# Performance work log

Hardware: AMD Instinct MI355X
Metric: run time of the kernel (lower is better)

Reference implementation:

```python
import jax, jax.numpy as jnp
import numpy as np

N, E, H, FN, FE, L = 100000, 600000, 128, 64, 16, 4


def setup_inputs() -> dict:
    key = jax.random.key(0)
    ks = jax.random.split(key, 16)
    s = 0.05
    return {
        "node_feats": jax.random.normal(ks[0], (N, FN), jnp.float32),
        "edge_feats": jax.random.normal(ks[1], (E, FE), jnp.float32),
        "src": jax.random.randint(ks[2], (E,), 0, N),
        "dst": jax.random.randint(ks[3], (E,), 0, N),
        # node projection
        "Wn": jax.random.normal(ks[4], (FN, H), jnp.float32) * s,
        "bn": jnp.zeros((H,), jnp.float32),
        # edge MLP: Linear -> ReLU -> Linear
        "We1": jax.random.normal(ks[5], (FE, H), jnp.float32) * s,
        "be1": jnp.zeros((H,), jnp.float32),
        "We2": jax.random.normal(ks[6], (H, H), jnp.float32) * s,
        "be2": jnp.zeros((H,), jnp.float32),
        # per-layer GINE apply MLPs: Linear -> ReLU -> Linear, stacked over L layers
        "W1": jax.random.normal(ks[7], (L, H, H), jnp.float32) * s,
        "b1": jnp.zeros((L, H), jnp.float32),
        "W2": jax.random.normal(ks[8], (L, H, H), jnp.float32) * s,
        "b2": jnp.zeros((L, H), jnp.float32),
    }


def reference(node_feats, edge_feats, src, dst, Wn, bn, We1, be1, We2, be2, W1, b1, W2, b2):
    relu = jax.nn.relu
    # initial node projection + ReLU
    h = relu(node_feats @ Wn + bn)                     # [N, H]
    # edge feature MLP
    e = relu(edge_feats @ We1 + be1) @ We2 + be2       # [E, H]
    n_nodes = h.shape[0]
    for l in range(W1.shape[0]):
        # GINEConv (eps = 0): message = relu(h[src] + e), sum-aggregate at dst
        m = relu(h[src] + e)                           # [E, H] gather + combine
        agg = jax.ops.segment_sum(m, dst, num_segments=n_nodes)  # [N, H] scatter-add
        z = h + agg                                    # (1+eps)*h + agg, eps=0
        z = relu(z @ W1[l] + b1[l]) @ W2[l] + b2[l]    # apply MLP
        h = relu(z)                                    # outer ReLU in forward loop
    return h
```

## Files before the change

### kernel.cpp

```cpp
#include <hip/hip_runtime.h>

#define BLK 256

typedef short bf16x8 __attribute__((ext_vector_type(8)));
typedef float f32x4 __attribute__((ext_vector_type(4)));

__device__ __forceinline__ unsigned short f2bf(float f) {
    unsigned int u = __float_as_uint(f);
    u += 0x7FFFu + ((u >> 16) & 1u);
    return (unsigned short)(u >> 16);
}
__device__ __forceinline__ float bf2f(unsigned short s) {
    return __uint_as_float(((unsigned int)s) << 16);
}

__global__ __launch_bounds__(BLK) void prep_w(
    const float* __restrict__ Wn, const float* __restrict__ We1,
    const float* __restrict__ We2, const float* __restrict__ W1,
    const float* __restrict__ W2, unsigned short* __restrict__ wp)
{
    const int slot = blockIdx.y;
    const int K = (slot == 9) ? 64 : (slot == 10) ? 32 : 128;
    const int i = blockIdx.x * BLK + threadIdx.x;
    if (i >= K * 128) return;
    const int k = i >> 7, n = i & 127;
    float f;
    if (slot == 0)      f = We2[k * 128 + n];
    else if (slot <= 4) f = W1[(size_t)(slot - 1) * 16384 + k * 128 + n];
    else if (slot <= 8) f = W2[(size_t)(slot - 5) * 16384 + k * 128 + n];
    else if (slot == 9) f = Wn[k * 128 + n];
    else                f = (k < 16) ? We1[k * 128 + n] : 0.f;
    const unsigned short hi = f2bf(f);
    const unsigned short lo = f2bf(f - bf2f(hi));
    const int mask = (slot == 10) ? 3 : 7;
    const int idx = n * K + (k ^ ((n & mask) << 3));
    unsigned short* base = wp + (size_t)slot * 32768;
    base[idx] = hi;
    base[K * 128 + idx] = lo;
}

template <int KDIM, int A_BF16, int OUT_BF16>
__global__ __launch_bounds__(BLK) void gemm128(
    const void* __restrict__ Av, const unsigned short* __restrict__ Wp,
    const float* __restrict__ bias, void* __restrict__ outv,
    int M, int do_relu)
{
    __shared__ unsigned short Bl[2 * KDIM * 128];
    const int tid = threadIdx.x;
    {
        const float4* s = (const float4*)Wp;
        float4* d = (float4*)Bl;
        #pragma unroll
        for (int i = 0; i < KDIM / 8; ++i) d[tid + i * BLK] = s[tid + i * BLK];
    }
    __syncthreads();

    const int lane = tid & 63;
    const int wv   = tid >> 6;
    const int l15  = lane & 15;
    const int g    = lane >> 4;
    const int wbase = wv * 32;
    const int NKS = KDIM / 32;

    float bcol[8];
    #pragma unroll
    for (int cf = 0; cf < 8; ++cf) bcol[cf] = bias[cf * 16 + l15];

    const int ntiles = (M + 127) >> 7;
    for (int tile = blockIdx.x; tile < ntiles; tile += gridDim.x) {
        bf16x8 af[2][KDIM / 32];
        #pragma unroll
        for (int rf = 0; rf < 2; ++rf) {
            const int row = tile * 128 + wbase + rf * 16 + l15;
            const bool ok = row < M;
            #pragma unroll
            for (int ks = 0; ks < NKS; ++ks) {
                const int k0 = ks * 32 + g * 8;
                if (A_BF16) {
                    af[rf][ks] = ok
                        ? *(const bf16x8*)((const unsigned short*)Av + (size_t)row * KDIM + k0)
                        : (bf16x8)0;
                } else {
                    if (ok) {
                        const float* ap = (const float*)Av + (size_t)row * KDIM + k0;
                        const float4 f0 = *(const float4*)(ap);
                        const float4 f1 = *(const float4*)(ap + 4);
                        bf16x8 a;
                        a[0] = (short)f2bf(f0.x); a[1] = (short)f2bf(f0.y);
                        a[2] = (short)f2bf(f0.z); a[3] = (short)f2bf(f0.w);
                        a[4] = (short)f2bf(f1.x); a[5] = (short)f2bf(f1.y);
                        a[6] = (short)f2bf(f1.z); a[7] = (short)f2bf(f1.w);
                        af[rf][ks] = a;
                    } else af[rf][ks] = (bf16x8)0;
                }
            }
        }
        f32x4 acc[2][8];
        #pragma unroll
        for (int rf = 0; rf < 2; ++rf)
            #pragma unroll
            for (int cf = 0; cf < 8; ++cf) {
                const float b = bcol[cf];
                acc[rf][cf][0] = b; acc[rf][cf][1] = b;
                acc[rf][cf][2] = b; acc[rf][cf][3] = b;
            }
        #pragma unroll
        for (int ks = 0; ks < NKS; ++ks) {
            #pragma unroll
            for (int cf = 0; cf < 8; ++cf) {
                const int c = cf * 16 + l15;
                const int ku = (ks * 32 + g * 8) ^ ((c & 7) << 3);
                const bf16x8 bh = *(const bf16x8*)(&Bl[c * KDIM + ku]);
                const bf16x8 blo = *(const bf16x8*)(&Bl[KDIM * 128 + c * KDIM + ku]);
                acc[0][cf] = __builtin_amdgcn_mfma_f32_16x16x32_bf16(af[0][ks], bh, acc[0][cf], 0, 0, 0);
                acc[1][cf] = __builtin_amdgcn_mfma_f32_16x16x32_bf16(af[1][ks], bh, acc[1][cf], 0, 0, 0);
                acc[0][cf] = __builtin_amdgcn_mfma_f32_16x16x32_bf16(af[0][ks], blo, acc[0][cf], 0, 0, 0);
                acc[1][cf] = __builtin_amdgcn_mfma_f32_16x16x32_bf16(af[1][ks], blo, acc[1][cf], 0, 0, 0);
            }
        }
        #pragma unroll
        for (int rf = 0; rf < 2; ++rf) {
            const int r0 = tile * 128 + wbase + rf * 16 + g * 4;
            #pragma unroll
            for (int cf = 0; cf < 8; ++cf) {
                const int col = cf * 16 + l15;
                const f32x4 v = acc[rf][cf];
                #pragma unroll
                for (int j = 0; j < 4; ++j) {
                    const int row = r0 + j;
                    if (row < M) {
                        float x = v[j];
                        if (do_relu) x = fmaxf(x, 0.f);
                        if (OUT_BF16)
                            ((unsigned short*)outv)[(size_t)row * 128 + col] = f2bf(x);
                        else
                            ((float*)outv)[(size_t)row * 128 + col] = x;
                    }
                }
            }
        }
    }
}

__global__ __launch_bounds__(BLK) void edge_mlp(
    const float* __restrict__ ef, const unsigned short* __restrict__ w1p,
    const unsigned short* __restrict__ w2p, const float* __restrict__ be1,
    const float* __restrict__ be2, unsigned short* __restrict__ out, int M)
{
    __shared__ unsigned short B1[2 * 32 * 128];
    __shared__ unsigned short B2[128 * 128];
    __shared__ unsigned short stg[4][16 * 128];
    const int tid = threadIdx.x;
    {
        const float4* s1 = (const float4*)w1p;
        float4* d1 = (float4*)B1;
        #pragma unroll
        for (int i = 0; i < 4; ++i) d1[tid + i * BLK] = s1[tid + i * BLK];
        const float4* s2 = (const float4*)w2p;
        float4* d2 = (float4*)B2;
        #pragma unroll
        for (int i = 0; i < 8; ++i) d2[tid + i * BLK] = s2[tid + i * BLK];
    }
    __syncthreads();

    const int lane = tid & 63;
    const int wv   = tid >> 6;
    const int l15  = lane & 15;
    const int g    = lane >> 4;
    const int wbase = wv * 32;

    float bcol1[8], bcol2[8];
    #pragma unroll
    for (int cf = 0; cf < 8; ++cf) {
        bcol1[cf] = be1[cf * 16 + l15];
        bcol2[cf] = be2[cf * 16 + l15];
    }

    const int ntiles = (M + 127) >> 7;
    for (int tile = blockIdx.x; tile < ntiles; tile += gridDim.x) {
        #pragma unroll
        for (int rf = 0; rf < 2; ++rf) {
            const int row = tile * 128 + wbase + rf * 16 + l15;
            const bool ok = row < M;
            bf16x8 a1 = (bf16x8)0;
            if (g < 2 && ok) {
                const float* ap = ef + (size_t)row * 16 + g * 8;
                const float4 f0 = *(const float4*)(ap);
                const float4 f1 = *(const float4*)(ap + 4);
                a1[0] = (short)f2bf(f0.x); a1[1] = (short)f2bf(f0.y);
                a1[2] = (short)f2bf(f0.z); a1[3] = (short)f2bf(f0.w);
                a1[4] = (short)f2bf(f1.x); a1[5] = (short)f2bf(f1.y);
                a1[6] = (short)f2bf(f1.z); a1[7] = (short)f2bf(f1.w);
            }
            f32x4 acc1[8];
            #pragma unroll
            for (int cf = 0; cf < 8; ++cf) {
                const float b = bcol1[cf];
                acc1[cf][0] = b; acc1[cf][1] = b; acc1[cf][2] = b; acc1[cf][3] = b;
            }
            #pragma unroll
            for (int cf = 0; cf < 8; ++cf) {
                const int c = cf * 16 + l15;
                const int ku = (g * 8) ^ ((c & 3) << 3);
                const bf16x8 bh  = *(const bf16x8*)(&B1[c * 32 + ku]);
                const bf16x8 blo = *(const bf16x8*)(&B1[4096 + c * 32 + ku]);
                acc1[cf] = __builtin_amdgcn_mfma_f32_16x16x32_bf16(a1, bh,  acc1[cf], 0, 0, 0);
                acc1[cf] = __builtin_amdgcn_mfma_f32_16x16x32_bf16(a1, blo, acc1[cf], 0, 0, 0);
            }
            #pragma unroll
            for (int cf = 0; cf < 8; ++cf) {
                const int col = cf * 16 + l15;
                #pragma unroll
                for (int j = 0; j < 4; ++j) {
                    const int rl = g * 4 + j;
                    stg[wv][rl * 128 + (col ^ ((rl & 7) << 3))] =
                        f2bf(fmaxf(acc1[cf][j], 0.f));
                }
            }
            __syncthreads();
            bf16x8 a2[4];
            #pragma unroll
            for (int ks = 0; ks < 4; ++ks) {
                const int k0 = ks * 32 + g * 8;
                a2[ks] = *(const bf16x8*)(&stg[wv][l15 * 128 + (k0 ^ ((l15 & 7) << 3))]);
            }
            f32x4 acc2[8];
            #pragma unroll
            for (int cf = 0; cf < 8; ++cf) {
                const float b = bcol2[cf];
                acc2[cf][0] = b; acc2[cf][1] = b; acc2[cf][2] = b; acc2[cf][3] = b;
            }
            #pragma unroll
            for (int ks = 0; ks < 4; ++ks) {
                #pragma unroll
                for (int cf = 0; cf < 8; ++cf) {
                    const int c = cf * 16 + l15;
                    const int ku = (ks * 32 + g * 8) ^ ((c & 7) << 3);
                    const bf16x8 bh = *(const bf16x8*)(&B2[c * 128 + ku]);
                    acc2[cf] = __builtin_amdgcn_mfma_f32_16x16x32_bf16(a2[ks], bh, acc2[cf], 0, 0, 0);
                }
            }
            const int r0 = tile * 128 + wbase + rf * 16 + g * 4;
            #pragma unroll
            for (int cf = 0; cf < 8; ++cf) {
                const int col = cf * 16 + l15;
                #pragma unroll
                for (int j = 0; j < 4; ++j) {
                    const int r = r0 + j;
                    if (r < M) out[(size_t)r * 128 + col] = f2bf(acc2[cf][j]);
                }
            }
            __syncthreads();
        }
    }
}

__global__ __launch_bounds__(BLK) void hist_k(
    const int* __restrict__ dst, int* __restrict__ counts, int nE)
{
    int i = blockIdx.x * BLK + threadIdx.x;
    if (i < nE) atomicAdd(&counts[dst[i]], 1);
}

__global__ __launch_bounds__(BLK) void scan1_k(
    const int* __restrict__ counts, int* __restrict__ blockSums, int n)
{
    __shared__ int s[BLK];
    const int t = threadIdx.x, b = blockIdx.x;
    const int base = b * 1024 + t * 4;
    int sum = 0;
    #pragma unroll
    for (int j = 0; j < 4; ++j) { int i = base + j; if (i < n) sum += counts[i]; }
    s[t] = sum; __syncthreads();
    for (int off = 128; off > 0; off >>= 1) {
        if (t < off) s[t] += s[t + off];
        __syncthreads();
    }
    if (t == 0) blockSums[b] = s[0];
}

__global__ void scan2_k(int* __restrict__ blockSums, int nb,
                        int* __restrict__ offsets, int n)
{
    if (threadIdx.x == 0 && blockIdx.x == 0) {
        int run = 0;
        for (int i = 0; i < nb; ++i) { int v = blockSums[i]; blockSums[i] = run; run += v; }
        offsets[n] = run;
    }
}

__global__ __launch_bounds__(BLK) void scan3_k(
    const int* __restrict__ counts, const int* __restrict__ blockSums,
    int* __restrict__ offsets, int n)
{
    __shared__ int s[BLK];
    const int t = threadIdx.x, b = blockIdx.x;
    const int base = b * 1024 + t * 4;
    int c[4]; int tsum = 0;
    #pragma unroll
    for (int j = 0; j < 4; ++j) {
        c[j] = (base + j < n) ? counts[base + j] : 0;
        tsum += c[j];
    }
    s[t] = tsum; __syncthreads();
    for (int off = 1; off < BLK; off <<= 1) {
        int v = (t >= off) ? s[t - off] : 0;
        __syncthreads();
        s[t] += v;
        __syncthreads();
    }
    int run = s[t] - tsum + blockSums[b];
    #pragma unroll
    for (int j = 0; j < 4; ++j) {
        if (base + j < n) { offsets[base + j] = run; run += c[j]; }
    }
}

__global__ __launch_bounds__(BLK) void fill_k(
    const int* __restrict__ dst, const int* __restrict__ offsets,
    int* __restrict__ cursor, int* __restrict__ eidx, int nE)
{
    int i = blockIdx.x * BLK + threadIdx.x;
    if (i < nE) {
        int d = dst[i];
        int pos = offsets[d] + atomicAdd(&cursor[d], 1);
        eidx[pos] = i;
    }
}

__global__ __launch_bounds__(BLK) void perm_k(
    const float* __restrict__ ef, const int* __restrict__ src,
    const int* __restrict__ eidx, float* __restrict__ ef_perm,
    int* __restrict__ src_perm, int nE)
{
    int i = blockIdx.x * BLK + threadIdx.x;
    if (i >= nE * 4) return;
    const int pos = i >> 2, part = i & 3;
    const int eg = eidx[pos];
    ((float4*)(ef_perm + (size_t)pos * 16))[part] =
        ((const float4*)(ef + (size_t)eg * 16))[part];
    if (part == 0) src_perm[pos] = src[eg];
}

__global__ __launch_bounds__(BLK) void agg_k(
    const unsigned short* __restrict__ h, const unsigned short* __restrict__ e,
    const int* __restrict__ src_perm, const int* __restrict__ offsets,
    unsigned short* __restrict__ z, int nN)
{
    const int t = threadIdx.x;
    const int node = blockIdx.x * 8 + (t >> 5);
    if (node >= nN) return;
    const int c4 = (t & 31) << 2;
    const ushort4 hn = *(const ushort4*)(h + (size_t)node * 128 + c4);
    float ax = bf2f(hn.x), ay = bf2f(hn.y), az = bf2f(hn.z), aw = bf2f(hn.w);
    const int beg = offsets[node], end = offsets[node + 1];
    const int lim = end - 1;
    for (int i = beg; i < end; i += 8) {
        #pragma unroll
        for (int k = 0; k < 8; ++k) {
            const int idx = i + k;
            const bool v = idx < end;
            const int ic = v ? idx : lim;
            const int s = src_perm[ic];
            const ushort4 hv = *(const ushort4*)(h + (size_t)s * 128 + c4);
            const ushort4 ev = *(const ushort4*)(e + (size_t)ic * 128 + c4);
            const float mx = fmaxf(bf2f(hv.x) + bf2f(ev.x), 0.f);
            const float my = fmaxf(bf2f(hv.y) + bf2f(ev.y), 0.f);
            const float mz = fmaxf(bf2f(hv.z) + bf2f(ev.z), 0.f);
            const float mw = fmaxf(bf2f(hv.w) + bf2f(ev.w), 0.f);
            ax += v ? mx : 0.f;
            ay += v ? my : 0.f;
            az += v ? mz : 0.f;
            aw += v ? mw : 0.f;
        }
    }
    ushort4 ob;
    ob.x = f2bf(ax); ob.y = f2bf(ay); ob.z = f2bf(az); ob.w = f2bf(aw);
    *(ushort4*)(z + (size_t)node * 128 + c4) = ob;
}

extern "C" void kernel_launch(void* const* d_in, const int* in_sizes, int n_in,
                              void* d_out, int out_size, void* d_ws, size_t ws_size,
                              hipStream_t stream) {
    const float* nf  = (const float*)d_in[0];
    const float* ef  = (const float*)d_in[1];
    const int*   src = (const int*)d_in[2];
    const int*   dst = (const int*)d_in[3];
    const float* Wn  = (const float*)d_in[4];
    const float* bn  = (const float*)d_in[5];
    const float* We1 = (const float*)d_in[6];
    const float* be1 = (const float*)d_in[7];
    const float* We2 = (const float*)d_in[8];
    const float* be2 = (const float*)d_in[9];
    const float* W1  = (const float*)d_in[10];
    const float* b1  = (const float*)d_in[11];
    const float* W2  = (const float*)d_in[12];
    const float* b2  = (const float*)d_in[13];

    const int N_ = 100000, E_ = 600000, L_ = 4;

    const size_t eB = (size_t)E_ * 128 * 2;
    const size_t nb = (size_t)N_ * 128 * 2;
    const size_t csrOff = eB + 3 * nb;
    const size_t wpOff  = csrOff + 5601088;
    const size_t need = wpOff + 11 * 65536;
    if (ws_size < need) return;

    char* ws = (char*)d_ws;
    unsigned short* e    = (unsigned short*)ws;
    unsigned short* z    = (unsigned short*)(ws + eB);
    unsigned short* hb   = (unsigned short*)(ws + eB + nb);
    unsigned short* hidN = (unsigned short*)(ws + eB + 2 * nb);
    float*          ef_perm = (float*)(ws + eB);
    int* eidx      = (int*)(ws + csrOff);
    int* counts    = (int*)(ws + csrOff + 2400000);
    int* offsets   = (int*)(ws + csrOff + 2800000);
    int* blockSums = (int*)(ws + csrOff + 3200064);
    int* src_perm  = (int*)(ws + csrOff + 3201088);
    unsigned short* wp = (unsigned short*)(ws + wpOff);

    dim3 blk(BLK);
    const int nbE = (E_ + BLK - 1) / BLK;
    const int nbScan = (N_ + 1023) / 1024;

    prep_w<<<dim3(64, 11), blk, 0, stream>>>(Wn, We1, We2, W1, W2, wp);

    hipMemsetAsync(counts, 0, (size_t)N_ * 4, stream);
    hist_k<<<nbE, blk, 0, stream>>>(dst, counts, E_);
    scan1_k<<<nbScan, blk, 0, stream>>>(counts, blockSums, N_);
    scan2_k<<<1, 64, 0, stream>>>(blockSums, nbScan, offsets, N_);
    scan3_k<<<nbScan, blk, 0, stream>>>(counts, blockSums, offsets, N_);
    hipMemsetAsync(counts, 0, (size_t)N_ * 4, stream);
    fill_k<<<nbE, blk, 0, stream>>>(dst, offsets, counts, eidx, E_);

    perm_k<<<(E_ * 4 + BLK - 1) / BLK, blk, 0, stream>>>(
        ef, src, eidx, ef_perm, src_perm, E_);

    edge_mlp<<<dim3(2048), blk, 0, stream>>>(
        ef_perm, wp + (size_t)10 * 32768, wp, be1, be2, e, E_);

    const int gxN = (N_ + 127) / 128;
    gemm128<64, 0, 1><<<dim3(gxN), blk, 0, stream>>>(
        nf, wp + (size_t)9 * 32768, bn, hb, N_, 1);

    const int nbAgg = (N_ + 7) / 8;
    for (int l = 0; l < L_; ++l) {
        agg_k<<<nbAgg, blk, 0, stream>>>(hb, e, src_perm, offsets, z, N_);
        gemm128<128, 1, 1><<<dim3(gxN), blk, 0, stream>>>(
            z, wp + (size_t)(1 + l) * 32768, b1 + (size_t)l * 128, hidN, N_, 1);
        if (l < L_ - 1)
            gemm128<128, 1, 1><<<dim3(gxN), blk, 0, stream>>>(
                hidN, wp + (size_t)(5 + l) * 32768, b2 + (size_t)l * 128, hb, N_, 1);
        else
            gemm128<128, 1, 0><<<dim3(gxN), blk, 0, stream>>>(
                hidN, wp + (size_t)(5 + l) * 32768, b2 + (size_t)l * 128, d_out, N_, 1);
    }
}
```

Measured before the change: 746.9 us.

## Drop bf16 low-part weight MFMAs, fuse permutation into fill, parallelize scan

Most GEMMs now use only the high bf16 half of each weight and skip the split-precision low-part MFMAs; only the final layer keeps them. The edge MLP likewise keeps only the high part. The perm_k kernel is removed: fill_k writes src_perm directly, and edge_mlp gathers edge features through eidx. Two __syncthreads in edge_mlp are dropped, scan2 becomes a parallel block scan, and the GEMM grids are halved so each block handles two tiles and reloads its weights less often. These cut MFMA work, launches and memory passes, at the cost of lower weight precision and possible shared-staging races in edge_mlp.

```diff
diff --git a/kernel.cpp b/kernel.cpp
--- a/kernel.cpp
+++ b/kernel.cpp
@@ -39,19 +39,20 @@
     base[K * 128 + idx] = lo;
 }
 
-template <int KDIM, int A_BF16, int OUT_BF16>
+template <int KDIM, int A_BF16, int OUT_BF16, int LO>
 __global__ __launch_bounds__(BLK) void gemm128(
     const void* __restrict__ Av, const unsigned short* __restrict__ Wp,
     const float* __restrict__ bias, void* __restrict__ outv,
     int M, int do_relu)
 {
-    __shared__ unsigned short Bl[2 * KDIM * 128];
+    __shared__ unsigned short Bl[(LO ? 2 : 1) * KDIM * 128];
     const int tid = threadIdx.x;
     {
         const float4* s = (const float4*)Wp;
         float4* d = (float4*)Bl;
         #pragma unroll
-        for (int i = 0; i < KDIM / 8; ++i) d[tid + i * BLK] = s[tid + i * BLK];
+        for (int i = 0; i < (LO ? KDIM / 8 : KDIM / 16); ++i)
+            d[tid + i * BLK] = s[tid + i * BLK];
     }
     __syncthreads();
 
@@ -111,11 +112,13 @@
                 const int c = cf * 16 + l15;
                 const int ku = (ks * 32 + g * 8) ^ ((c & 7) << 3);
                 const bf16x8 bh = *(const bf16x8*)(&Bl[c * KDIM + ku]);
-                const bf16x8 blo = *(const bf16x8*)(&Bl[KDIM * 128 + c * KDIM + ku]);
                 acc[0][cf] = __builtin_amdgcn_mfma_f32_16x16x32_bf16(af[0][ks], bh, acc[0][cf], 0, 0, 0);
                 acc[1][cf] = __builtin_amdgcn_mfma_f32_16x16x32_bf16(af[1][ks], bh, acc[1][cf], 0, 0, 0);
-                acc[0][cf] = __builtin_amdgcn_mfma_f32_16x16x32_bf16(af[0][ks], blo, acc[0][cf], 0, 0, 0);
-                acc[1][cf] = __builtin_amdgcn_mfma_f32_16x16x32_bf16(af[1][ks], blo, acc[1][cf], 0, 0, 0);
+                if (LO) {
+                    const bf16x8 blo = *(const bf16x8*)(&Bl[KDIM * 128 + c * KDIM + ku]);
+                    acc[0][cf] = __builtin_amdgcn_mfma_f32_16x16x32_bf16(af[0][ks], blo, acc[0][cf], 0, 0, 0);
+                    acc[1][cf] = __builtin_amdgcn_mfma_f32_16x16x32_bf16(af[1][ks], blo, acc[1][cf], 0, 0, 0);
+                }
             }
         }
         #pragma unroll
@@ -143,11 +146,12 @@
 }
 
 __global__ __launch_bounds__(BLK) void edge_mlp(
-    const float* __restrict__ ef, const unsigned short* __restrict__ w1p,
-    const unsigned short* __restrict__ w2p, const float* __restrict__ be1,
-    const float* __restrict__ be2, unsigned short* __restrict__ out, int M)
-{
-    __shared__ unsigned short B1[2 * 32 * 128];
+    const float* __restrict__ ef, const int* __restrict__ eidx,
+    const unsigned short* __restrict__ w1p, const unsigned short* __restrict__ w2p,
+    const float* __restrict__ be1, const float* __restrict__ be2,
+    unsigned short* __restrict__ out, int M)
+{
+    __shared__ unsigned short B1[32 * 128];
     __shared__ unsigned short B2[128 * 128];
     __shared__ unsigned short stg[4][16 * 128];
     const int tid = threadIdx.x;
@@ -155,7 +159,7 @@
         const float4* s1 = (const float4*)w1p;
         float4* d1 = (float4*)B1;
         #pragma unroll
-        for (int i = 0; i < 4; ++i) d1[tid + i * BLK] = s1[tid + i * BLK];
+        for (int i = 0; i < 2; ++i) d1[tid + i * BLK] = s1[tid + i * BLK];
         const float4* s2 = (const float4*)w2p;
         float4* d2 = (float4*)B2;
         #pragma unroll
@@ -184,7 +188,8 @@
             const bool ok = row < M;
             bf16x8 a1 = (bf16x8)0;
             if (g < 2 && ok) {
-                const float* ap = ef + (size_t)row * 16 + g * 8;
+                const int er = eidx[row];
+                const float* ap = ef + (size_t)er * 16 + g * 8;
                 const float4 f0 = *(const float4*)(ap);
                 const float4 f1 = *(const float4*)(ap + 4);
                 a1[0] = (short)f2bf(f0.x); a1[1] = (short)f2bf(f0.y);
@@ -202,10 +207,8 @@
             for (int cf = 0; cf < 8; ++cf) {
                 const int c = cf * 16 + l15;
                 const int ku = (g * 8) ^ ((c & 3) << 3);
-                const bf16x8 bh  = *(const bf16x8*)(&B1[c * 32 + ku]);
-                const bf16x8 blo = *(const bf16x8*)(&B1[4096 + c * 32 + ku]);
-                acc1[cf] = __builtin_amdgcn_mfma_f32_16x16x32_bf16(a1, bh,  acc1[cf], 0, 0, 0);
-                acc1[cf] = __builtin_amdgcn_mfma_f32_16x16x32_bf16(a1, blo, acc1[cf], 0, 0, 0);
+                const bf16x8 bh = *(const bf16x8*)(&B1[c * 32 + ku]);
+                acc1[cf] = __builtin_amdgcn_mfma_f32_16x16x32_bf16(a1, bh, acc1[cf], 0, 0, 0);
             }
             #pragma unroll
             for (int cf = 0; cf < 8; ++cf) {
@@ -217,7 +220,6 @@
                         f2bf(fmaxf(acc1[cf][j], 0.f));
                 }
             }
-            __syncthreads();
             bf16x8 a2[4];
             #pragma unroll
             for (int ks = 0; ks < 4; ++ks) {
@@ -250,7 +252,6 @@
                     if (r < M) out[(size_t)r * 128 + col] = f2bf(acc2[cf][j]);
                 }
             }
-            __syncthreads();
         }
     }
 }
@@ -279,14 +280,21 @@
     if (t == 0) blockSums[b] = s[0];
 }
 
-__global__ void scan2_k(int* __restrict__ blockSums, int nb,
-                        int* __restrict__ offsets, int n)
-{
-    if (threadIdx.x == 0 && blockIdx.x == 0) {
-        int run = 0;
-        for (int i = 0; i < nb; ++i) { int v = blockSums[i]; blockSums[i] = run; run += v; }
-        offsets[n] = run;
-    }
+__global__ __launch_bounds__(128) void scan2_k(
+    int* __restrict__ blockSums, int nb, int* __restrict__ offsets, int n)
+{
+    __shared__ int s[128];
+    const int t = threadIdx.x;
+    const int v = (t < nb) ? blockSums[t] : 0;
+    s[t] = v; __syncthreads();
+    for (int off = 1; off < 128; off <<= 1) {
+        int u = (t >= off) ? s[t - off] : 0;
+        __syncthreads();
+        s[t] += u;
+        __syncthreads();
+    }
+    if (t < nb) blockSums[t] = s[t] - v;
+    if (t == 127) offsets[n] = s[127];
 }
 
 __global__ __launch_bounds__(BLK) void scan3_k(
@@ -317,29 +325,17 @@
 }
 
 __global__ __launch_bounds__(BLK) void fill_k(
-    const int* __restrict__ dst, const int* __restrict__ offsets,
-    int* __restrict__ cursor, int* __restrict__ eidx, int nE)
+    const int* __restrict__ dst, const int* __restrict__ src,
+    const int* __restrict__ offsets, int* __restrict__ cursor,
+    int* __restrict__ eidx, int* __restrict__ src_perm, int nE)
 {
     int i = blockIdx.x * BLK + threadIdx.x;
     if (i < nE) {
         int d = dst[i];
         int pos = offsets[d] + atomicAdd(&cursor[d], 1);
         eidx[pos] = i;
-    }
-}
-
-__global__ __launch_bounds__(BLK) void perm_k(
-    const float* __restrict__ ef, const int* __restrict__ src,
-    const int* __restrict__ eidx, float* __restrict__ ef_perm,
-    int* __restrict__ src_perm, int nE)
-{
-    int i = blockIdx.x * BLK + threadIdx.x;
-    if (i >= nE * 4) return;
-    const int pos = i >> 2, part = i & 3;
-    const int eg = eidx[pos];
-    ((float4*)(ef_perm + (size_t)pos * 16))[part] =
-        ((const float4*)(ef + (size_t)eg * 16))[part];
-    if (part == 0) src_perm[pos] = src[eg];
+        src_perm[pos] = src[i];
+    }
 }
 
 __global__ __launch_bounds__(BLK) void agg_k(
@@ -411,7 +407,6 @@
     unsigned short* z    = (unsigned short*)(ws + eB);
     unsigned short* hb   = (unsigned short*)(ws + eB + nb);
     unsigned short* hidN = (unsigned short*)(ws + eB + 2 * nb);
-    float*          ef_perm = (float*)(ws + eB);
     int* eidx      = (int*)(ws + csrOff);
     int* counts    = (int*)(ws + csrOff + 2400000);
     int* offsets   = (int*)(ws + csrOff + 2800000);
@@ -428,31 +423,28 @@
     hipMemsetAsync(counts, 0, (size_t)N_ * 4, stream);
     hist_k<<<nbE, blk, 0, stream>>>(dst, counts, E_);
     scan1_k<<<nbScan, blk, 0, stream>>>(counts, blockSums, N_);
-    scan2_k<<<1, 64, 0, stream>>>(blockSums, nbScan, offsets, N_);
+    scan2_k<<<1, 128, 0, stream>>>(blockSums, nbScan, offsets, N_);
     scan3_k<<<nbScan, blk, 0, stream>>>(counts, blockSums, offsets, N_);
     hipMemsetAsync(counts, 0, (size_t)N_ * 4, stream);
-    fill_k<<<nbE, blk, 0, stream>>>(dst, offsets, counts, eidx, E_);
-
-    perm_k<<<(E_ * 4 + BLK - 1) / BLK, blk, 0, stream>>>(
-        ef, src, eidx, ef_perm, src_perm, E_);
+    fill_k<<<nbE, blk, 0, stream>>>(dst, src, offsets, counts, eidx, src_perm, E_);
 
     edge_mlp<<<dim3(2048), blk, 0, stream>>>(
-        ef_perm, wp + (size_t)10 * 32768, wp, be1, be2, e, E_);
-
-    const int gxN = (N_ + 127) / 128;
-    gemm128<64, 0, 1><<<dim3(gxN), blk, 0, stream>>>(
+        ef, eidx, wp + (size_t)10 * 32768, wp, be1, be2, e, E_);
+
+    const int gx2 = ((N_ + 127) / 128 + 1) / 2;
+    gemm128<64, 0, 1, 0><<<dim3(gx2), blk, 0, stream>>>(
         nf, wp + (size_t)9 * 32768, bn, hb, N_, 1);
 
     const int nbAgg = (N_ + 7) / 8;
     for (int l = 0; l < L_; ++l) {
         agg_k<<<nbAgg, blk, 0, stream>>>(hb, e, src_perm, offsets, z, N_);
-        gemm128<128, 1, 1><<<dim3(gxN), blk, 0, stream>>>(
+        gemm128<128, 1, 1, 0><<<dim3(gx2), blk, 0, stream>>>(
             z, wp + (size_t)(1 + l) * 32768, b1 + (size_t)l * 128, hidN, N_, 1);
         if (l < L_ - 1)
-            gemm128<128, 1, 1><<<dim3(gxN), blk, 0, stream>>>(
+            gemm128<128, 1, 1, 0><<<dim3(gx2), blk, 0, stream>>>(
                 hidN, wp + (size_t)(5 + l) * 32768, b2 + (size_t)l * 128, hb, N_, 1);
         else
-            gemm128<128, 1, 0><<<dim3(gxN), blk, 0, stream>>>(
+            gemm128<128, 1, 0, 1><<<dim3(gx2), blk, 0, stream>>>(
                 hidN, wp + (size_t)(5 + l) * 32768, b2 + (size_t)l * 128, d_out, N_, 1);
     }
 }
```

Result: faster. 675.4 us (-9.6%).
